# Kernel tuning notes

Measured on AMD Instinct MI355X. Metric: run time of the kernel, lower is better.

## Reference

```python
import jax, jax.numpy as jnp
import numpy as np

N_NODES = 10000
N_EDGES = 160000
HIDDEN = 256
HEADS = 8
LN_EPS = 1e-5


def setup_inputs() -> dict:
    key = jax.random.key(0)
    ks = jax.random.split(key, 8)
    s = 1.0 / np.sqrt(HIDDEN)
    return {
        "node_embeddings": jax.random.normal(ks[0], (1, N_NODES, HIDDEN), jnp.float32),
        "edge_index": jax.random.randint(ks[1], (2, N_EDGES), 0, N_NODES, dtype=jnp.int32),
        "Wq": jax.random.normal(ks[2], (HIDDEN, HIDDEN), jnp.float32) * s,
        "Wk": jax.random.normal(ks[3], (HIDDEN, HIDDEN), jnp.float32) * s,
        "Wv": jax.random.normal(ks[4], (HIDDEN, HIDDEN), jnp.float32) * s,
        "Wo": jax.random.normal(ks[5], (HIDDEN, HIDDEN), jnp.float32) * s,
        "ln_gamma": jnp.ones((HIDDEN,), jnp.float32),
        "ln_beta": jnp.zeros((HIDDEN,), jnp.float32),
    }


def reference(node_embeddings, edge_index, Wq, Wk, Wv, Wo, ln_gamma, ln_beta):
    B, N, Dm = node_embeddings.shape
    H = HEADS
    hd = Dm // H
    scale = 1.0 / np.sqrt(hd)

    def heads(x):  # [B,N,Dm] -> [B,H,N,hd]
        return x.reshape(B, N, H, hd).transpose(0, 2, 1, 3)

    Q = heads(node_embeddings @ Wq)
    K = heads(node_embeddings @ Wk)
    V = heads(node_embeddings @ Wv)

    src, dst = edge_index[0], edge_index[1]
    Qe = Q[:, :, src, :]           # [B,H,E,hd]
    Ke = K[:, :, dst, :]
    Ve = V[:, :, dst, :]

    scores = jnp.einsum('bhed,bhed->bhe', Qe, Ke) * scale   # [B,H,E]
    s_t = scores.transpose(2, 0, 1)                          # [E,B,H]
    smax = jax.ops.segment_max(s_t, src, num_segments=N)    # [N,B,H]
    ex = jnp.exp(s_t - smax[src])                            # [E,B,H]
    denom = jax.ops.segment_sum(ex, src, num_segments=N)    # [N,B,H]
    attn = ex / denom[src]                                   # scatter-softmax weights

    wV = attn[..., None] * Ve.transpose(2, 0, 1, 3)          # [E,B,H,hd]
    agg = jax.ops.segment_sum(wV, src, num_segments=N)      # [N,B,H,hd]
    attn_out = agg.transpose(1, 0, 2, 3).reshape(B, N, Dm)   # [B,N,Dm]

    out = attn_out @ Wo
    x = out + node_embeddings
    mu = jnp.mean(x, axis=-1, keepdims=True)
    var = jnp.mean((x - mu) ** 2, axis=-1, keepdims=True)
    return (x - mu) * jax.lax.rsqrt(var + LN_EPS) * ln_gamma + ln_beta
```

## Files before the change

### kernel.cpp

```cpp
#include <hip/hip_runtime.h>

#define NN 10000
#define NE 160000
#define DM 256
#define CAP 96
#define LN_EPSF 1e-5f
#define SCALEF 0.17677669529663687f

typedef unsigned short u16;
typedef __attribute__((ext_vector_type(4))) u16 u16x4;
typedef __attribute__((ext_vector_type(8))) u16 u16x8;
typedef __attribute__((ext_vector_type(4))) float f32x4;
typedef __attribute__((ext_vector_type(8))) short short8;

__device__ __forceinline__ float b2f(u16 u) { return __uint_as_float(((unsigned)u) << 16); }
__device__ __forceinline__ u16 f2b(float f) {
    unsigned u = __float_as_uint(f);
    return (u16)((u + 0x7fffu + ((u >> 16) & 1u)) >> 16);
}
__device__ __forceinline__ int clampi(int v) { return v < 0 ? 0 : (v >= NN ? NN - 1 : v); }

__global__ void k_fill_zero_f32(float* __restrict__ o, int n) {
    int i = blockIdx.x * 256 + threadIdx.x;
    if (i < n) o[i] = 0.f;
}

__global__ void k_prep(const float* __restrict__ Wq, const float* __restrict__ Wk,
                       const float* __restrict__ Wv, const float* __restrict__ Wo,
                       u16* __restrict__ Wt, int* __restrict__ cnt) {
    int id = blockIdx.x * 256 + threadIdx.x;
    if (id < NN) cnt[id] = 0;
    int m = id >> 16;
    int rc = id & 65535;
    int r = rc >> 8, c = rc & 255;
    const float* W = (m == 0) ? Wq : (m == 1) ? Wk : (m == 2) ? Wv : Wo;
    Wt[m * 65536 + c * 256 + r] = f2b(W[r * 256 + c]);
}

__global__ __launch_bounds__(256) void k_qkv_bucket(const float* __restrict__ X, const u16* __restrict__ Wt,
                                                    u16* __restrict__ Q, u16* __restrict__ KV,
                                                    const int* __restrict__ EI, int* __restrict__ cnt,
                                                    int* __restrict__ buck) {
    constexpr int AS = 40;
    __shared__ u16 At[64 * AS];
    __shared__ u16 Bt[256 * AS];
    if (blockIdx.y == 3) {
        int e = blockIdx.x * 256 + threadIdx.x;
        if (e < NE) {
            int s = clampi(EI[e]);
            int slot = atomicAdd(&cnt[s], 1);
            if (slot < CAP) buck[s * CAP + slot] = clampi(EI[NE + e]);
        }
        return;
    }
    if (blockIdx.x >= 157) return;
    const int t = threadIdx.x;
    const int w = t >> 6, l = t & 63, quad = l >> 4, m16 = l & 15;
    const int mat = blockIdx.y;
    const u16* Wm = Wt + mat * 65536;
    const int node0 = blockIdx.x * 64;
    f32x4 acc[16];
#pragma unroll
    for (int i = 0; i < 16; i++) acc[i] = (f32x4){0.f, 0.f, 0.f, 0.f};
    const int arow = t >> 2, ac8 = (t & 3) * 8;
    for (int k0 = 0; k0 < DM; k0 += 32) {
        u16x8 av = {0, 0, 0, 0, 0, 0, 0, 0};
        int anode = node0 + arow;
        if (anode < NN) {
            const float* xp = X + (size_t)anode * DM + k0 + ac8;
            f32x4 a0 = *(const f32x4*)(xp);
            f32x4 a1 = *(const f32x4*)(xp + 4);
            av[0] = f2b(a0[0]); av[1] = f2b(a0[1]); av[2] = f2b(a0[2]); av[3] = f2b(a0[3]);
            av[4] = f2b(a1[0]); av[5] = f2b(a1[1]); av[6] = f2b(a1[2]); av[7] = f2b(a1[3]);
        }
        *(u16x8*)(At + arow * AS + ac8) = av;
        const u16* bsrc = Wm + t * DM + k0;
        u16x8 b0 = *(const u16x8*)(bsrc);
        u16x8 b1 = *(const u16x8*)(bsrc + 8);
        u16x8 b2 = *(const u16x8*)(bsrc + 16);
        u16x8 b3 = *(const u16x8*)(bsrc + 24);
        u16* bd = Bt + t * AS;
        *(u16x8*)(bd) = b0;
        *(u16x8*)(bd + 8) = b1;
        *(u16x8*)(bd + 16) = b2;
        *(u16x8*)(bd + 24) = b3;
        __syncthreads();
        short8 a = *(const short8*)(At + (w * 16 + m16) * AS + quad * 8);
#pragma unroll
        for (int ct = 0; ct < 16; ct++) {
            short8 b = *(const short8*)(Bt + (ct * 16 + m16) * AS + quad * 8);
            acc[ct] = __builtin_amdgcn_mfma_f32_16x16x32_bf16(a, b, acc[ct], 0, 0, 0);
        }
        __syncthreads();
    }
#pragma unroll
    for (int ct = 0; ct < 16; ct++) {
        int col = ct * 16 + m16;
#pragma unroll
        for (int r = 0; r < 4; r++) {
            int node = node0 + w * 16 + quad * 4 + r;
            if (node < NN) {
                u16 v = f2b(acc[ct][r]);
                if (mat == 0) Q[(size_t)node * DM + col] = v;
                else KV[(size_t)node * 512 + (col >> 2) * 8 + (col & 3) + ((mat == 2) ? 4 : 0)] = v;
            }
        }
    }
}

__global__ __launch_bounds__(256) void k_edge(const u16* __restrict__ Q, const u16* __restrict__ KV,
                                              const int* __restrict__ cnt, const int* __restrict__ buck,
                                              u16* __restrict__ attn) {
    const int t = threadIdx.x;
    const int w = t >> 6, l = t & 63;
    const int node = blockIdx.x * 4 + w;
    const int d0 = l * 4;
    int deg = cnt[node];
    if (deg > CAP) deg = CAP;
    const int* bl = buck + node * CAP;
    u16x4 q4 = *(const u16x4*)(Q + (size_t)node * DM + d0);
    float qf0 = b2f(q4[0]) * SCALEF, qf1 = b2f(q4[1]) * SCALEF;
    float qf2 = b2f(q4[2]) * SCALEF, qf3 = b2f(q4[3]) * SCALEF;
    float m = -3.0e38f, s = 0.f;
    float a0 = 0.f, a1 = 0.f, a2 = 0.f, a3 = 0.f;
    for (int i = 0; i < deg; i++) {
        int dst = bl[i];
        u16x8 kv = *(const u16x8*)(KV + (size_t)dst * 512 + l * 8);
        float p = qf0 * b2f(kv[0]) + qf1 * b2f(kv[1]) + qf2 * b2f(kv[2]) + qf3 * b2f(kv[3]);
        p += __shfl_xor(p, 1, 64);
        p += __shfl_xor(p, 2, 64);
        p += __shfl_xor(p, 4, 64);
        float nm = fmaxf(m, p);
        float al = __expf(m - nm);
        float pe = __expf(p - nm);
        s = s * al + pe;
        a0 = a0 * al + pe * b2f(kv[4]);
        a1 = a1 * al + pe * b2f(kv[5]);
        a2 = a2 * al + pe * b2f(kv[6]);
        a3 = a3 * al + pe * b2f(kv[7]);
        m = nm;
    }
    float inv = (s > 0.f) ? 1.f / s : 0.f;
    u16x4 o;
    o[0] = f2b(a0 * inv);
    o[1] = f2b(a1 * inv);
    o[2] = f2b(a2 * inv);
    o[3] = f2b(a3 * inv);
    *(u16x4*)(attn + (size_t)node * DM + d0) = o;
}

__global__ __launch_bounds__(256) void k_gemm_out_ln(const u16* __restrict__ In, const u16* __restrict__ WoT,
                                                     const float* __restrict__ X, const float* __restrict__ g,
                                                     const float* __restrict__ b, float* __restrict__ out) {
    constexpr int AS = 40;
    __shared__ u16 At[64 * AS];
    __shared__ u16 Bt[256 * AS];
    __shared__ float gl[256], bl[256];
    const int t = threadIdx.x;
    gl[t] = g[t];
    bl[t] = b[t];
    const int w = t >> 6, l = t & 63, quad = l >> 4, m16 = l & 15;
    const int node0 = blockIdx.x * 64;
    f32x4 acc[16];
#pragma unroll
    for (int i = 0; i < 16; i++) acc[i] = (f32x4){0.f, 0.f, 0.f, 0.f};
    const int arow = t >> 2, ac8 = (t & 3) * 8;
    for (int k0 = 0; k0 < DM; k0 += 32) {
        u16x8 av = {0, 0, 0, 0, 0, 0, 0, 0};
        int anode = node0 + arow;
        if (anode < NN) av = *(const u16x8*)(In + (size_t)anode * DM + k0 + ac8);
        *(u16x8*)(At + arow * AS + ac8) = av;
        const u16* bsrc = WoT + t * DM + k0;
        u16x8 b0 = *(const u16x8*)(bsrc);
        u16x8 b1 = *(const u16x8*)(bsrc + 8);
        u16x8 b2 = *(const u16x8*)(bsrc + 16);
        u16x8 b3 = *(const u16x8*)(bsrc + 24);
        u16* bd = Bt + t * AS;
        *(u16x8*)(bd) = b0;
        *(u16x8*)(bd + 8) = b1;
        *(u16x8*)(bd + 16) = b2;
        *(u16x8*)(bd + 24) = b3;
        __syncthreads();
        short8 a = *(const short8*)(At + (w * 16 + m16) * AS + quad * 8);
#pragma unroll
        for (int ct = 0; ct < 16; ct++) {
            short8 bfr = *(const short8*)(Bt + (ct * 16 + m16) * AS + quad * 8);
            acc[ct] = __builtin_amdgcn_mfma_f32_16x16x32_bf16(a, bfr, acc[ct], 0, 0, 0);
        }
        __syncthreads();
    }
    float val[16][4];
    const int nodeBase = node0 + w * 16 + quad * 4;
#pragma unroll
    for (int ct = 0; ct < 16; ct++) {
        int col = ct * 16 + m16;
#pragma unroll
        for (int r = 0; r < 4; r++) {
            int node = nodeBase + r;
            float x = (node < NN) ? X[(size_t)node * DM + col] : 0.f;
            val[ct][r] = acc[ct][r] + x;
        }
    }
    float mu[4], rstd[4];
#pragma unroll
    for (int r = 0; r < 4; r++) {
        float s1 = 0.f, s2 = 0.f;
#pragma unroll
        for (int ct = 0; ct < 16; ct++) {
            float v = val[ct][r];
            s1 += v;
            s2 += v * v;
        }
#pragma unroll
        for (int o = 1; o < 16; o <<= 1) {
            s1 += __shfl_xor(s1, o, 64);
            s2 += __shfl_xor(s2, o, 64);
        }
        float mm = s1 * (1.f / DM);
        float var = s2 * (1.f / DM) - mm * mm;
        mu[r] = mm;
        rstd[r] = rsqrtf(var + LN_EPSF);
    }
#pragma unroll
    for (int ct = 0; ct < 16; ct++) {
        int col = ct * 16 + m16;
#pragma unroll
        for (int r = 0; r < 4; r++) {
            int node = nodeBase + r;
            if (node < NN)
                out[(size_t)node * DM + col] = (val[ct][r] - mu[r]) * rstd[r] * gl[col] + bl[col];
        }
    }
}

extern "C" void kernel_launch(void* const* d_in, const int* in_sizes, int n_in,
                              void* d_out, int out_size, void* d_ws, size_t ws_size,
                              hipStream_t stream) {
    (void)in_sizes; (void)n_in;
    const float* X  = (const float*)d_in[0];
    const int*   EI = (const int*)d_in[1];
    const float* Wq = (const float*)d_in[2];
    const float* Wk = (const float*)d_in[3];
    const float* Wv = (const float*)d_in[4];
    const float* Wo = (const float*)d_in[5];
    const float* g  = (const float*)d_in[6];
    const float* be = (const float*)d_in[7];

    const size_t SWT  = (size_t)4 * 65536 * 2;
    const size_t SKV  = (size_t)NN * 512 * 2;
    const size_t SAT  = (size_t)NN * DM * 2;
    const size_t SCNT = (size_t)NN * 4;
    const size_t SBK  = (size_t)NN * CAP * 4;
    const size_t need = SWT + SKV + SAT + SCNT + SBK;
    if (ws_size < need) {
        k_fill_zero_f32<<<(out_size + 255) / 256, 256, 0, stream>>>((float*)d_out, out_size);
        return;
    }
    char* p = (char*)d_ws;
    u16* Wt   = (u16*)p; p += SWT;
    u16* KVb  = (u16*)p; p += SKV;
    u16* attn = (u16*)p; p += SAT;
    int* cnt  = (int*)p; p += SCNT;
    int* buck = (int*)p; p += SBK;
    u16* Qb = (u16*)d_out;

    k_prep<<<1024, 256, 0, stream>>>(Wq, Wk, Wv, Wo, Wt, cnt);
    k_qkv_bucket<<<dim3(625, 4), 256, 0, stream>>>(X, Wt, Qb, KVb, EI, cnt, buck);
    k_edge<<<NN / 4, 256, 0, stream>>>(Qb, KVb, cnt, buck, attn);
    k_gemm_out_ln<<<157, 256, 0, stream>>>(attn, Wt + 3 * 65536, X, g, be, (float*)d_out);
}
```

Before: 153.3 us.

## Retile GEMM waves to 64x64 subtiles and unroll edge softmax loop by four

Both GEMM kernels now give each wave a 64x64 output subtile, with four row and four column MFMA fragments. Previously each wave owned 16 rows across all 256 columns, so each wave loaded 17 fragments from LDS per k-step; it now loads 8, cutting LDS traffic. Because a node's row now spans several waves, the LayerNorm epilogue does a cross-wave reduction through shared memory with extra barriers. The edge kernel processes four neighbours per iteration with independent online-softmax states merged at the end, exposing more memory-level parallelism on the gathered K/V loads at the cost of more registers and exp operations.

```diff
diff --git a/kernel.cpp b/kernel.cpp
--- a/kernel.cpp
+++ b/kernel.cpp
@@ -59,9 +59,11 @@
     const int mat = blockIdx.y;
     const u16* Wm = Wt + mat * 65536;
     const int node0 = blockIdx.x * 64;
-    f32x4 acc[16];
-#pragma unroll
-    for (int i = 0; i < 16; i++) acc[i] = (f32x4){0.f, 0.f, 0.f, 0.f};
+    f32x4 acc[4][4];
+#pragma unroll
+    for (int i = 0; i < 4; i++)
+#pragma unroll
+        for (int j = 0; j < 4; j++) acc[i][j] = (f32x4){0.f, 0.f, 0.f, 0.f};
     const int arow = t >> 2, ac8 = (t & 3) * 8;
     for (int k0 = 0; k0 < DM; k0 += 32) {
         u16x8 av = {0, 0, 0, 0, 0, 0, 0, 0};
@@ -85,28 +87,49 @@
         *(u16x8*)(bd + 16) = b2;
         *(u16x8*)(bd + 24) = b3;
         __syncthreads();
-        short8 a = *(const short8*)(At + (w * 16 + m16) * AS + quad * 8);
-#pragma unroll
-        for (int ct = 0; ct < 16; ct++) {
-            short8 b = *(const short8*)(Bt + (ct * 16 + m16) * AS + quad * 8);
-            acc[ct] = __builtin_amdgcn_mfma_f32_16x16x32_bf16(a, b, acc[ct], 0, 0, 0);
-        }
+        short8 a[4], b[4];
+#pragma unroll
+        for (int rt = 0; rt < 4; rt++)
+            a[rt] = *(const short8*)(At + (rt * 16 + m16) * AS + quad * 8);
+#pragma unroll
+        for (int ct = 0; ct < 4; ct++)
+            b[ct] = *(const short8*)(Bt + (w * 64 + ct * 16 + m16) * AS + quad * 8);
+#pragma unroll
+        for (int rt = 0; rt < 4; rt++)
+#pragma unroll
+            for (int ct = 0; ct < 4; ct++)
+                acc[rt][ct] = __builtin_amdgcn_mfma_f32_16x16x32_bf16(a[rt], b[ct], acc[rt][ct], 0, 0, 0);
         __syncthreads();
     }
 #pragma unroll
-    for (int ct = 0; ct < 16; ct++) {
-        int col = ct * 16 + m16;
-#pragma unroll
-        for (int r = 0; r < 4; r++) {
-            int node = node0 + w * 16 + quad * 4 + r;
-            if (node < NN) {
-                u16 v = f2b(acc[ct][r]);
-                if (mat == 0) Q[(size_t)node * DM + col] = v;
-                else KV[(size_t)node * 512 + (col >> 2) * 8 + (col & 3) + ((mat == 2) ? 4 : 0)] = v;
-            }
-        }
-    }
-}
+    for (int rt = 0; rt < 4; rt++) {
+#pragma unroll
+        for (int ct = 0; ct < 4; ct++) {
+            int col = w * 64 + ct * 16 + m16;
+#pragma unroll
+            for (int r = 0; r < 4; r++) {
+                int node = node0 + rt * 16 + quad * 4 + r;
+                if (node < NN) {
+                    u16 v = f2b(acc[rt][ct][r]);
+                    if (mat == 0) Q[(size_t)node * DM + col] = v;
+                    else KV[(size_t)node * 512 + (col >> 2) * 8 + (col & 3) + ((mat == 2) ? 4 : 0)] = v;
+                }
+            }
+        }
+    }
+}
+
+#define UPD(mm, ss, AA, kv, p) do {                  \
+    float nm_ = fmaxf(mm, p);                        \
+    float al_ = __expf(mm - nm_);                    \
+    float pe_ = __expf(p - nm_);                     \
+    ss = ss * al_ + pe_;                             \
+    AA[0] = AA[0] * al_ + pe_ * b2f(kv[4]);          \
+    AA[1] = AA[1] * al_ + pe_ * b2f(kv[5]);          \
+    AA[2] = AA[2] * al_ + pe_ * b2f(kv[6]);          \
+    AA[3] = AA[3] * al_ + pe_ * b2f(kv[7]);          \
+    mm = nm_;                                        \
+} while (0)
 
 __global__ __launch_bounds__(256) void k_edge(const u16* __restrict__ Q, const u16* __restrict__ KV,
                                               const int* __restrict__ cnt, const int* __restrict__ buck,
@@ -121,31 +144,52 @@
     u16x4 q4 = *(const u16x4*)(Q + (size_t)node * DM + d0);
     float qf0 = b2f(q4[0]) * SCALEF, qf1 = b2f(q4[1]) * SCALEF;
     float qf2 = b2f(q4[2]) * SCALEF, qf3 = b2f(q4[3]) * SCALEF;
-    float m = -3.0e38f, s = 0.f;
-    float a0 = 0.f, a1 = 0.f, a2 = 0.f, a3 = 0.f;
-    for (int i = 0; i < deg; i++) {
+    float m0 = -3.0e38f, m1 = -3.0e38f, m2 = -3.0e38f, m3 = -3.0e38f;
+    float s0 = 0.f, s1 = 0.f, s2 = 0.f, s3 = 0.f;
+    f32x4 A0 = {0.f, 0.f, 0.f, 0.f}, A1 = {0.f, 0.f, 0.f, 0.f};
+    f32x4 A2 = {0.f, 0.f, 0.f, 0.f}, A3 = {0.f, 0.f, 0.f, 0.f};
+    int i = 0;
+    int deg4 = deg & ~3;
+    for (; i < deg4; i += 4) {
+        int4 e4 = *(const int4*)(bl + i);
+        u16x8 kv0 = *(const u16x8*)(KV + (size_t)e4.x * 512 + l * 8);
+        u16x8 kv1 = *(const u16x8*)(KV + (size_t)e4.y * 512 + l * 8);
+        u16x8 kv2 = *(const u16x8*)(KV + (size_t)e4.z * 512 + l * 8);
+        u16x8 kv3 = *(const u16x8*)(KV + (size_t)e4.w * 512 + l * 8);
+        float p0 = qf0 * b2f(kv0[0]) + qf1 * b2f(kv0[1]) + qf2 * b2f(kv0[2]) + qf3 * b2f(kv0[3]);
+        float p1 = qf0 * b2f(kv1[0]) + qf1 * b2f(kv1[1]) + qf2 * b2f(kv1[2]) + qf3 * b2f(kv1[3]);
+        float p2 = qf0 * b2f(kv2[0]) + qf1 * b2f(kv2[1]) + qf2 * b2f(kv2[2]) + qf3 * b2f(kv2[3]);
+        float p3 = qf0 * b2f(kv3[0]) + qf1 * b2f(kv3[1]) + qf2 * b2f(kv3[2]) + qf3 * b2f(kv3[3]);
+        p0 += __shfl_xor(p0, 1, 64); p1 += __shfl_xor(p1, 1, 64);
+        p2 += __shfl_xor(p2, 1, 64); p3 += __shfl_xor(p3, 1, 64);
+        p0 += __shfl_xor(p0, 2, 64); p1 += __shfl_xor(p1, 2, 64);
+        p2 += __shfl_xor(p2, 2, 64); p3 += __shfl_xor(p3, 2, 64);
+        p0 += __shfl_xor(p0, 4, 64); p1 += __shfl_xor(p1, 4, 64);
+        p2 += __shfl_xor(p2, 4, 64); p3 += __shfl_xor(p3, 4, 64);
+        UPD(m0, s0, A0, kv0, p0);
+        UPD(m1, s1, A1, kv1, p1);
+        UPD(m2, s2, A2, kv2, p2);
+        UPD(m3, s3, A3, kv3, p3);
+    }
+    for (; i < deg; ++i) {
         int dst = bl[i];
         u16x8 kv = *(const u16x8*)(KV + (size_t)dst * 512 + l * 8);
         float p = qf0 * b2f(kv[0]) + qf1 * b2f(kv[1]) + qf2 * b2f(kv[2]) + qf3 * b2f(kv[3]);
         p += __shfl_xor(p, 1, 64);
         p += __shfl_xor(p, 2, 64);
         p += __shfl_xor(p, 4, 64);
-        float nm = fmaxf(m, p);
-        float al = __expf(m - nm);
-        float pe = __expf(p - nm);
-        s = s * al + pe;
-        a0 = a0 * al + pe * b2f(kv[4]);
-        a1 = a1 * al + pe * b2f(kv[5]);
-        a2 = a2 * al + pe * b2f(kv[6]);
-        a3 = a3 * al + pe * b2f(kv[7]);
-        m = nm;
-    }
+        UPD(m0, s0, A0, kv, p);
+    }
+    float nm = fmaxf(fmaxf(m0, m1), fmaxf(m2, m3));
+    float w0 = __expf(m0 - nm), w1 = __expf(m1 - nm);
+    float w2 = __expf(m2 - nm), w3 = __expf(m3 - nm);
+    float s = s0 * w0 + s1 * w1 + s2 * w2 + s3 * w3;
     float inv = (s > 0.f) ? 1.f / s : 0.f;
     u16x4 o;
-    o[0] = f2b(a0 * inv);
-    o[1] = f2b(a1 * inv);
-    o[2] = f2b(a2 * inv);
-    o[3] = f2b(a3 * inv);
+    o[0] = f2b((A0[0] * w0 + A1[0] * w1 + A2[0] * w2 + A3[0] * w3) * inv);
+    o[1] = f2b((A0[1] * w0 + A1[1] * w1 + A2[1] * w2 + A3[1] * w3) * inv);
+    o[2] = f2b((A0[2] * w0 + A1[2] * w1 + A2[2] * w2 + A3[2] * w3) * inv);
+    o[3] = f2b((A0[3] * w0 + A1[3] * w1 + A2[3] * w2 + A3[3] * w3) * inv);
     *(u16x4*)(attn + (size_t)node * DM + d0) = o;
 }
 
@@ -155,15 +199,19 @@
     constexpr int AS = 40;
     __shared__ u16 At[64 * AS];
     __shared__ u16 Bt[256 * AS];
-    __shared__ float gl[256], bl[256];
+    __shared__ float gbuf[256], bbuf[256];
+    __shared__ float redS[4][64], redQ[4][64];
+    __shared__ float muS[64], rsS[64];
     const int t = threadIdx.x;
-    gl[t] = g[t];
-    bl[t] = b[t];
+    gbuf[t] = g[t];
+    bbuf[t] = b[t];
     const int w = t >> 6, l = t & 63, quad = l >> 4, m16 = l & 15;
     const int node0 = blockIdx.x * 64;
-    f32x4 acc[16];
-#pragma unroll
-    for (int i = 0; i < 16; i++) acc[i] = (f32x4){0.f, 0.f, 0.f, 0.f};
+    f32x4 acc[4][4];
+#pragma unroll
+    for (int i = 0; i < 4; i++)
+#pragma unroll
+        for (int j = 0; j < 4; j++) acc[i][j] = (f32x4){0.f, 0.f, 0.f, 0.f};
     const int arow = t >> 2, ac8 = (t & 3) * 8;
     for (int k0 = 0; k0 < DM; k0 += 32) {
         u16x8 av = {0, 0, 0, 0, 0, 0, 0, 0};
@@ -181,56 +229,74 @@
         *(u16x8*)(bd + 16) = b2;
         *(u16x8*)(bd + 24) = b3;
         __syncthreads();
-        short8 a = *(const short8*)(At + (w * 16 + m16) * AS + quad * 8);
-#pragma unroll
-        for (int ct = 0; ct < 16; ct++) {
-            short8 bfr = *(const short8*)(Bt + (ct * 16 + m16) * AS + quad * 8);
-            acc[ct] = __builtin_amdgcn_mfma_f32_16x16x32_bf16(a, bfr, acc[ct], 0, 0, 0);
-        }
+        short8 a[4], bf[4];
+#pragma unroll
+        for (int rt = 0; rt < 4; rt++)
+            a[rt] = *(const short8*)(At + (rt * 16 + m16) * AS + quad * 8);
+#pragma unroll
+        for (int ct = 0; ct < 4; ct++)
+            bf[ct] = *(const short8*)(Bt + (w * 64 + ct * 16 + m16) * AS + quad * 8);
+#pragma unroll
+        for (int rt = 0; rt < 4; rt++)
+#pragma unroll
+            for (int ct = 0; ct < 4; ct++)
+                acc[rt][ct] = __builtin_amdgcn_mfma_f32_16x16x32_bf16(a[rt], bf[ct], acc[rt][ct], 0, 0, 0);
         __syncthreads();
     }
-    float val[16][4];
-    const int nodeBase = node0 + w * 16 + quad * 4;
-#pragma unroll
-    for (int ct = 0; ct < 16; ct++) {
-        int col = ct * 16 + m16;
+#pragma unroll
+    for (int rt = 0; rt < 4; rt++)
+#pragma unroll
+        for (int ct = 0; ct < 4; ct++) {
+            int col = w * 64 + ct * 16 + m16;
+#pragma unroll
+            for (int r = 0; r < 4; r++) {
+                int node = node0 + rt * 16 + quad * 4 + r;
+                float x = (node < NN) ? X[(size_t)node * DM + col] : 0.f;
+                acc[rt][ct][r] += x;
+            }
+        }
+#pragma unroll
+    for (int rt = 0; rt < 4; rt++) {
 #pragma unroll
         for (int r = 0; r < 4; r++) {
-            int node = nodeBase + r;
-            float x = (node < NN) ? X[(size_t)node * DM + col] : 0.f;
-            val[ct][r] = acc[ct][r] + x;
-        }
-    }
-    float mu[4], rstd[4];
-#pragma unroll
-    for (int r = 0; r < 4; r++) {
-        float s1 = 0.f, s2 = 0.f;
-#pragma unroll
-        for (int ct = 0; ct < 16; ct++) {
-            float v = val[ct][r];
-            s1 += v;
-            s2 += v * v;
-        }
-#pragma unroll
-        for (int o = 1; o < 16; o <<= 1) {
-            s1 += __shfl_xor(s1, o, 64);
-            s2 += __shfl_xor(s2, o, 64);
-        }
-        float mm = s1 * (1.f / DM);
-        float var = s2 * (1.f / DM) - mm * mm;
-        mu[r] = mm;
-        rstd[r] = rsqrtf(var + LN_EPSF);
-    }
-#pragma unroll
-    for (int ct = 0; ct < 16; ct++) {
-        int col = ct * 16 + m16;
-#pragma unroll
-        for (int r = 0; r < 4; r++) {
-            int node = nodeBase + r;
-            if (node < NN)
-                out[(size_t)node * DM + col] = (val[ct][r] - mu[r]) * rstd[r] * gl[col] + bl[col];
-        }
-    }
+            float p1 = acc[rt][0][r] + acc[rt][1][r] + acc[rt][2][r] + acc[rt][3][r];
+            float p2 = acc[rt][0][r] * acc[rt][0][r] + acc[rt][1][r] * acc[rt][1][r] +
+                       acc[rt][2][r] * acc[rt][2][r] + acc[rt][3][r] * acc[rt][3][r];
+#pragma unroll
+            for (int o = 1; o < 16; o <<= 1) {
+                p1 += __shfl_xor(p1, o, 64);
+                p2 += __shfl_xor(p2, o, 64);
+            }
+            if (m16 == 0) {
+                int row = rt * 16 + quad * 4 + r;
+                redS[w][row] = p1;
+                redQ[w][row] = p2;
+            }
+        }
+    }
+    __syncthreads();
+    if (t < 64) {
+        float s1t = redS[0][t] + redS[1][t] + redS[2][t] + redS[3][t];
+        float s2t = redQ[0][t] + redQ[1][t] + redQ[2][t] + redQ[3][t];
+        float mm = s1t * (1.f / DM);
+        float var = s2t * (1.f / DM) - mm * mm;
+        muS[t] = mm;
+        rsS[t] = rsqrtf(var + LN_EPSF);
+    }
+    __syncthreads();
+#pragma unroll
+    for (int rt = 0; rt < 4; rt++)
+#pragma unroll
+        for (int ct = 0; ct < 4; ct++) {
+            int col = w * 64 + ct * 16 + m16;
+#pragma unroll
+            for (int r = 0; r < 4; r++) {
+                int row = rt * 16 + quad * 4 + r;
+                int node = node0 + row;
+                if (node < NN)
+                    out[(size_t)node * DM + col] = (acc[rt][ct][r] - muS[row]) * rsS[row] * gbuf[col] + bbuf[col];
+            }
+        }
 }
 
 extern "C" void kernel_launch(void* const* d_in, const int* in_sizes, int n_in,
```

After: 143.7 us. 1.07x faster.
